# Performance work log

Measured on AMD Instinct MI355X. Metric: run time of the kernel, lower is better.

The kernel has to match this reference:

```python
import jax, jax.numpy as jnp
import numpy as np

B, NQ, NK = 16, 1024, 1024
DQ = DK = DV = 512
H = 4
DH = DV // H  # 128


def layer_norm(x, g, b, eps=1e-5):
    mu = jnp.mean(x, axis=-1, keepdims=True)
    var = jnp.var(x, axis=-1, keepdims=True)  # biased, matches torch LayerNorm
    return (x - mu) / jnp.sqrt(var + eps) * g + b


def setup_inputs() -> dict:
    key = jax.random.key(0)
    ks = jax.random.split(key, 16)
    s = lambda d: 1.0 / np.sqrt(d)
    return {
        "Q": jax.random.normal(ks[0], (B, NQ, DQ), jnp.float32),
        "K": jax.random.normal(ks[1], (B, NK, DK), jnp.float32),
        "weights": jax.random.uniform(ks[2], (H * B, NQ, NK), jnp.float32),
        "Wq": jax.random.normal(ks[3], (DV, DQ), jnp.float32) * s(DQ),
        "bq": jnp.zeros((DV,), jnp.float32),
        "Wk": jax.random.normal(ks[4], (DV, DK), jnp.float32) * s(DK),
        "bk": jnp.zeros((DV,), jnp.float32),
        "Wv": jax.random.normal(ks[5], (DV, DK), jnp.float32) * s(DK),
        "bv": jnp.zeros((DV,), jnp.float32),
        "Wo": jax.random.normal(ks[6], (DV, DV), jnp.float32) * s(DV),
        "bo": jnp.zeros((DV,), jnp.float32),
        "g0": jnp.ones((DV,), jnp.float32),
        "beta0": jnp.zeros((DV,), jnp.float32),
        "g1": jnp.ones((DV,), jnp.float32),
        "beta1": jnp.zeros((DV,), jnp.float32),
    }


def reference(Q, K, weights, Wq, bq, Wk, bk, Wv, bv, Wo, bo, g0, beta0, g1, beta1):
    q = Q @ Wq.T + bq  # [B,NQ,DV]
    k = K @ Wk.T + bk  # [B,NK,DV]
    v = K @ Wv.T + bv  # [B,NK,DV]

    # torch split(dh, 2) + cat(0) == head-major [H,B,N,DH]
    def heads(x, n):
        return x.reshape(B, n, H, DH).transpose(2, 0, 1, 3)

    q_, k_, v_ = heads(q, NQ), heads(k, NK), heads(v, NK)

    # NOTE: original scales by sqrt(dim_V), not sqrt(head_dim)
    scores = jnp.einsum("hbqd,hbkd->hbqk", q_, k_) / np.sqrt(DV)
    log_w = jnp.log(jnp.clip(weights, 0.0, None)).reshape(H, B, NQ, NK)
    A = jax.nn.softmax(scores + log_w, axis=-1)  # [H,B,NQ,NK]

    o = q_ + jnp.einsum("hbqk,hbkd->hbqd", A, v_)  # residual inside heads
    # split(B,0)+cat(2) == merge heads back to [B,NQ,DV]
    O = o.transpose(1, 2, 0, 3).reshape(B, NQ, DV)
    O = layer_norm(O, g0, beta0)
    O = O + jax.nn.relu(O @ Wo.T + bo)
    O = layer_norm(O, g1, beta1)
    return O
```

## Files before the change

kernel.cpp:

```cpp
#include <hip/hip_runtime.h>

typedef unsigned short u16;
typedef unsigned int u32;
typedef __attribute__((ext_vector_type(8))) short short8;
typedef __attribute__((ext_vector_type(4))) float f32x4;
typedef __attribute__((ext_vector_type(2))) u32 uintx2;
typedef __attribute__((address_space(3))) u32 lds32;
typedef const __attribute__((address_space(1))) u32 g32c;

__device__ __forceinline__ u16 f2bf(float f) {
  union { float f; u32 u; } v; v.f = f;
  return (u16)((v.u + 0x7fffu + ((v.u >> 16) & 1u)) >> 16);
}
__device__ __forceinline__ float bf2f(u16 h) {
  union { u32 u; float f; } v; v.u = ((u32)h) << 16;
  return v.f;
}

__global__ void cvt_w_kernel(const float* __restrict__ Wq, const float* __restrict__ Wk,
                             const float* __restrict__ Wv, const float* __restrict__ Wo,
                             u16* __restrict__ dst) {
  int m = blockIdx.y;
  const float* s = (m == 0) ? Wq : (m == 1) ? Wk : (m == 2) ? Wv : Wo;
  int idx = (blockIdx.x * 256 + threadIdx.x) * 4;
  float4 v = *(const float4*)(s + idx);
  uintx2 pk;
  pk[0] = (u32)f2bf(v.x) | ((u32)f2bf(v.y) << 16);
  pk[1] = (u32)f2bf(v.z) | ((u32)f2bf(v.w) << 16);
  *(uintx2*)(dst + m * 262144 + idx) = pk;
}

template <bool AF32, bool OUTMODE, bool TRANSV>
__device__ __forceinline__ void gemm_bt_body(const void* __restrict__ Ap,
                                             const u16* __restrict__ Bw,
                                             const float* __restrict__ bias,
                                             u16* __restrict__ C) {
  __shared__ u16 ldsA[128 * 64];
  __shared__ u16 ldsB[128 * 64];
  const int t = threadIdx.x;
  const int lane = t & 63, wid = t >> 6;
  const int lr = lane & 15, lg = lane >> 4;
  const int n0 = blockIdx.x * 128;
  const int m0 = blockIdx.y * 128;
  const int wr = (wid >> 1) * 64, wc = (wid & 1) * 64;

  f32x4 acc[4][4];
#pragma unroll
  for (int i = 0; i < 4; ++i)
#pragma unroll
    for (int j = 0; j < 4; ++j)
#pragma unroll
      for (int r = 0; r < 4; ++r) acc[i][j][r] = 0.f;

  for (int kt = 0; kt < 512; kt += 64) {
    __syncthreads();
#pragma unroll
    for (int i = 0; i < 4; ++i) {
      int lin = i * 256 + t;
      int row = lin >> 3, u = lin & 7;
      int pu = u ^ (row & 7);
      if constexpr (AF32) {
        const float* src = (const float*)Ap + (size_t)(m0 + row) * 512 + kt + u * 8;
        float4 v0 = *(const float4*)src;
        float4 v1 = *(const float4*)(src + 4);
        short8 pk;
        pk[0] = (short)f2bf(v0.x); pk[1] = (short)f2bf(v0.y);
        pk[2] = (short)f2bf(v0.z); pk[3] = (short)f2bf(v0.w);
        pk[4] = (short)f2bf(v1.x); pk[5] = (short)f2bf(v1.y);
        pk[6] = (short)f2bf(v1.z); pk[7] = (short)f2bf(v1.w);
        *(short8*)&ldsA[row * 64 + pu * 8] = pk;
      } else {
        const u16* src = (const u16*)Ap + (size_t)(m0 + row) * 512 + kt + u * 8;
        *(short8*)&ldsA[row * 64 + pu * 8] = *(const short8*)src;
      }
      const u16* bsrc = Bw + (size_t)(n0 + row) * 512 + kt + u * 8;
      *(short8*)&ldsB[row * 64 + pu * 8] = *(const short8*)bsrc;
    }
    __syncthreads();
#pragma unroll
    for (int kk = 0; kk < 2; ++kk) {
      short8 af[4], bfr[4];
#pragma unroll
      for (int mf = 0; mf < 4; ++mf) {
        int row = wr + mf * 16 + lr;
        af[mf] = *(const short8*)&ldsA[row * 64 + (((kk * 4 + lg) ^ (row & 7)) * 8)];
      }
#pragma unroll
      for (int nf = 0; nf < 4; ++nf) {
        int row = wc + nf * 16 + lr;
        bfr[nf] = *(const short8*)&ldsB[row * 64 + (((kk * 4 + lg) ^ (row & 7)) * 8)];
      }
#pragma unroll
      for (int mf = 0; mf < 4; ++mf)
#pragma unroll
        for (int nf = 0; nf < 4; ++nf)
          acc[mf][nf] =
              __builtin_amdgcn_mfma_f32_16x16x32_bf16(af[mf], bfr[nf], acc[mf][nf], 0, 0, 0);
    }
  }

  if constexpr (TRANSV) {
    const int h_ = n0 >> 7;
#pragma unroll
    for (int mf = 0; mf < 4; ++mf)
#pragma unroll
      for (int nf = 0; nf < 4; ++nf) {
        int d = wc + nf * 16 + lr;
        int rr0 = m0 + wr + mf * 16 + lg * 4;
        int b_ = rr0 >> 10;
        int k0 = rr0 & 1023;
        float bvv = bias[n0 + d];
        uintx2 pk;
        pk[0] = (u32)f2bf(acc[mf][nf][0] + bvv) | ((u32)f2bf(acc[mf][nf][1] + bvv) << 16);
        pk[1] = (u32)f2bf(acc[mf][nf][2] + bvv) | ((u32)f2bf(acc[mf][nf][3] + bvv) << 16);
        *(uintx2*)(C + (((size_t)b_ * 4 + h_) * 128 + d) * 1024 + k0) = pk;
      }
  } else {
#pragma unroll
    for (int mf = 0; mf < 4; ++mf)
#pragma unroll
      for (int nf = 0; nf < 4; ++nf) {
        int c = n0 + wc + nf * 16 + lr;
        float bv = bias[c];
#pragma unroll
        for (int r = 0; r < 4; ++r) {
          int rr = m0 + wr + mf * 16 + lg * 4 + r;
          float v = acc[mf][nf][r] + bv;
          if constexpr (OUTMODE) {
            v = v > 0.f ? v : 0.f;
            v += bf2f(((const u16*)Ap)[(size_t)rr * 512 + c]);
          }
          C[(size_t)rr * 512 + c] = f2bf(v);
        }
      }
  }
}

__global__ __launch_bounds__(256) void gemm3_kernel(const float* __restrict__ Q,
                                                    const float* __restrict__ K,
                                                    const u16* __restrict__ Wb,
                                                    const float* __restrict__ bq,
                                                    const float* __restrict__ bk,
                                                    const float* __restrict__ bv,
                                                    u16* qb, u16* kb, u16* vbT) {
  int z = blockIdx.z;
  if (z == 2) {
    gemm_bt_body<true, false, true>(K, Wb + 524288, bv, vbT);
  } else {
    const void* Ap = (z == 0) ? (const void*)Q : (const void*)K;
    const u16* Bw = Wb + z * 262144;
    const float* bias = (z == 0) ? bq : bk;
    u16* C = (z == 0) ? qb : kb;
    gemm_bt_body<true, false, false>(Ap, Bw, bias, C);
  }
}

__global__ __launch_bounds__(256) void gemmo_kernel(const u16* __restrict__ X,
                                                    const u16* __restrict__ Wb,
                                                    const float* __restrict__ bo,
                                                    u16* Z) {
  gemm_bt_body<false, true, false>(X, Wb, bo, Z);
}

__global__ __launch_bounds__(256, 3) void attn_kernel(const u16* __restrict__ qb,
                                                      const u16* __restrict__ kb,
                                                      const u16* __restrict__ vbT,
                                                      const float* __restrict__ Wt,
                                                      u16* __restrict__ Ob) {
  __shared__ __align__(16) u16 ldsK[2][32 * 128];
  __shared__ __align__(16) u16 ldsVT[2][128 * 32];
  __shared__ __align__(16) u16 ldsP[64 * 40];
  const int t = threadIdx.x;
  const int lane = t & 63, wid = t >> 6;
  const int lr = lane & 15, lg = lane >> 4;
  const int hb = blockIdx.y;
  const int b = hb & 15;
  const int h = hb >> 4;
  const int q0 = blockIdx.x * 64;
  const int wq = wid * 16;
  const size_t kvbase = ((size_t)b * 1024) * 512 + h * 128;
  const size_t vtbase = ((size_t)b * 4 + h) * 131072;
  const float SCALE = 0.044194173824159216f;

  const u16* ksrc[2];
  const u16* vtsrc[2];
#pragma unroll
  for (int i = 0; i < 2; ++i) {
    {
      int lin = i * 256 + t;
      int row = lin >> 4, u = lin & 15;
      ksrc[i] = kb + kvbase + (size_t)row * 512 + ((u ^ (row & 15)) * 8);
    }
    {
      int lin = i * 256 + t;
      int row = lin >> 2, u = lin & 3;
      vtsrc[i] = vbT + vtbase + (size_t)row * 1024 + ((u ^ (row & 3)) * 8);
    }
  }
  const int wslot = (t & 192) * 8;

#define STAGE(bu)                                                                           \
  do {                                                                                      \
    _Pragma("unroll") for (int i_ = 0; i_ < 2; ++i_) {                                      \
      __builtin_amdgcn_global_load_lds((g32c*)(ksrc[i_]),                                   \
                                       (lds32*)(&ldsK[bu][i_ * 2048 + wslot]), 16, 0, 0);   \
      __builtin_amdgcn_global_load_lds((g32c*)(vtsrc[i_]),                                  \
                                       (lds32*)(&ldsVT[bu][i_ * 2048 + wslot]), 16, 0, 0);  \
      ksrc[i_] += 16384;                                                \
      vtsrc[i_] += 32;                                                  \
    }                                                                                       \
  } while (0)

  const float* wp = Wt + ((size_t)hb * 1024 + q0 + wq + lr) * 1024 + lg * 4;

#define WLOADP(W)                        \
  do {                                   \
    W[0] = *(const f32x4*)(wp);          \
    W[1] = *(const f32x4*)(wp + 16);     \
    wp += 32;                            \
  } while (0)

  short8 qfr[4];
  {
    const u16* qp = qb + kvbase + (size_t)(q0 + wq + lr) * 512 + lg * 8;
#pragma unroll
    for (int ds = 0; ds < 4; ++ds) qfr[ds] = *(const short8*)(qp + ds * 32);
  }

  f32x4 oacc[8];
#pragma unroll
  for (int j = 0; j < 8; ++j)
#pragma unroll
    for (int r = 0; r < 4; ++r) oacc[j][r] = 0.f;
  float lacc = 0.f;

  auto tile_compute = [&](const u16* bK, const u16* bVT, const f32x4 (&W)[2]) {
    f32x4 sacc[2];
#pragma unroll
    for (int j = 0; j < 2; ++j)
#pragma unroll
      for (int r = 0; r < 4; ++r) sacc[j][r] = 0.f;

#pragma unroll
    for (int ds = 0; ds < 4; ++ds) {
      short8 kf[2];
#pragma unroll
      for (int mf = 0; mf < 2; ++mf) {
        int row = mf * 16 + lr;
        kf[mf] = *(const short8*)&bK[row * 128 + (((ds * 4 + lg) ^ (row & 15)) * 8)];
      }
      __builtin_amdgcn_s_setprio(1);
#pragma unroll
      for (int mf = 0; mf < 2; ++mf)
        sacc[mf] = __builtin_amdgcn_mfma_f32_16x16x32_bf16(kf[mf], qfr[ds], sacc[mf], 0, 0, 0);
      __builtin_amdgcn_s_setprio(0);
    }

    const int prow = wq + lr;
#pragma unroll
    for (int mf = 0; mf < 2; ++mf) {
      f32x4 w4 = W[mf];
      float p0 = w4[0] * __expf(sacc[mf][0] * SCALE);
      float p1 = w4[1] * __expf(sacc[mf][1] * SCALE);
      float p2 = w4[2] * __expf(sacc[mf][2] * SCALE);
      float p3 = w4[3] * __expf(sacc[mf][3] * SCALE);
      lacc += (p0 + p1) + (p2 + p3);
      uintx2 pk;
      pk[0] = (u32)f2bf(p0) | ((u32)f2bf(p1) << 16);
      pk[1] = (u32)f2bf(p2) | ((u32)f2bf(p3) << 16);
      *(uintx2*)((char*)ldsP + prow * 80 + mf * 32 + lg * 8) = pk;
    }

    short8 pa = *(const short8*)((const char*)ldsP + (wq + lr) * 80 + lg * 16);
    short8 vf[8];
#pragma unroll
    for (int nf = 0; nf < 8; ++nf) {
      int row = nf * 16 + lr;
      vf[nf] = *(const short8*)&bVT[row * 32 + ((lg ^ (row & 3)) * 8)];
    }
    __builtin_amdgcn_s_setprio(1);
#pragma unroll
    for (int nf = 0; nf < 8; ++nf)
      oacc[nf] = __builtin_amdgcn_mfma_f32_16x16x32_bf16(pa, vf[nf], oacc[nf], 0, 0, 0);
    __builtin_amdgcn_s_setprio(0);
  };

#define SCHED_FENCE() __builtin_amdgcn_sched_barrier(0)
#define WAITBAR(N)                                                 \
  do {                                                             \
    SCHED_FENCE();                                                 \
    asm volatile("s_waitcnt vmcnt(" #N ")" ::: "memory");          \
    __builtin_amdgcn_s_barrier();                                  \
    SCHED_FENCE();                                                 \
  } while (0)
#define BAR()                                                      \
  do {                                                             \
    SCHED_FENCE();                                                 \
    __builtin_amdgcn_s_barrier();                                  \
    SCHED_FENCE();                                                 \
  } while (0)

  f32x4 wA[2], wB[2];
  WLOADP(wA);
  STAGE(0);

  for (int it = 0; it < 16; ++it) {
    {
      STAGE(1);
      WLOADP(wB);
      WAITBAR(6);
      tile_compute(&ldsK[0][0], &ldsVT[0][0], wA);
      BAR();
    }
    {
      if (it < 15) {
        STAGE(0);
        WLOADP(wA);
        WAITBAR(6);
      } else {
        WAITBAR(0);
      }
      tile_compute(&ldsK[1][0], &ldsVT[1][0], wB);
      if (it < 15) BAR();
    }
  }

  float lred = lacc;
  lred += __shfl_xor(lred, 16);
  lred += __shfl_xor(lred, 32);

#pragma unroll
  for (int r = 0; r < 4; ++r) {
    float lv = __shfl(lred, (lane & 48) | (lg * 4 + r));
    float linv = 1.0f / lv;
    int qrow = q0 + wq + lg * 4 + r;
    size_t base = kvbase + (size_t)qrow * 512;
#pragma unroll
    for (int nf = 0; nf < 8; ++nf) {
      size_t idx = base + nf * 16 + lr;
      Ob[idx] = f2bf(bf2f(qb[idx]) + oacc[nf][r] * linv);
    }
  }
#undef STAGE
#undef WLOADP
#undef WAITBAR
#undef BAR
#undef SCHED_FENCE
}

template <bool F32OUT>
__global__ __launch_bounds__(256) void ln_kernel(const u16* __restrict__ in,
                                                 const float* __restrict__ g,
                                                 const float* __restrict__ be,
                                                 void* __restrict__ outp) {
  const int lane = threadIdx.x & 63, wid = threadIdx.x >> 6;
  const int row = blockIdx.x * 4 + wid;
  const u16* p = in + (size_t)row * 512 + lane * 8;
  short8 v = *(const short8*)p;
  float x[8];
  float s = 0.f, s2 = 0.f;
#pragma unroll
  for (int j = 0; j < 8; ++j) {
    x[j] = bf2f((u16)v[j]);
    s += x[j];
    s2 += x[j] * x[j];
  }
#pragma unroll
  for (int off = 1; off < 64; off <<= 1) {
    s += __shfl_xor(s, off);
    s2 += __shfl_xor(s2, off);
  }
  float mu = s * (1.f / 512.f);
  float var = s2 * (1.f / 512.f) - mu * mu;
  float rs = rsqrtf(var + 1e-5f);
  float4 ga = *(const float4*)(g + lane * 8);
  float4 gb = *(const float4*)(g + lane * 8 + 4);
  float4 ba = *(const float4*)(be + lane * 8);
  float4 bb = *(const float4*)(be + lane * 8 + 4);
  float gg[8] = {ga.x, ga.y, ga.z, ga.w, gb.x, gb.y, gb.z, gb.w};
  float bv[8] = {ba.x, ba.y, ba.z, ba.w, bb.x, bb.y, bb.z, bb.w};
  if constexpr (F32OUT) {
    float* out = (float*)outp + (size_t)row * 512 + lane * 8;
    float4 o0, o1;
    o0.x = (x[0] - mu) * rs * gg[0] + bv[0];
    o0.y = (x[1] - mu) * rs * gg[1] + bv[1];
    o0.z = (x[2] - mu) * rs * gg[2] + bv[2];
    o0.w = (x[3] - mu) * rs * gg[3] + bv[3];
    o1.x = (x[4] - mu) * rs * gg[4] + bv[4];
    o1.y = (x[5] - mu) * rs * gg[5] + bv[5];
    o1.z = (x[6] - mu) * rs * gg[6] + bv[6];
    o1.w = (x[7] - mu) * rs * gg[7] + bv[7];
    *(float4*)out = o0;
    *(float4*)(out + 4) = o1;
  } else {
    short8 o;
#pragma unroll
    for (int j = 0; j < 8; ++j) o[j] = (short)f2bf((x[j] - mu) * rs * gg[j] + bv[j]);
    *(short8*)((u16*)outp + (size_t)row * 512 + lane * 8) = o;
  }
}

extern "C" void kernel_launch(void* const* d_in, const int* in_sizes, int n_in,
                              void* d_out, int out_size, void* d_ws, size_t ws_size,
                              hipStream_t stream) {
  (void)in_sizes; (void)n_in; (void)out_size; (void)ws_size;
  const float* Q   = (const float*)d_in[0];
  const float* K   = (const float*)d_in[1];
  const float* Wt  = (const float*)d_in[2];
  const float* Wq  = (const float*)d_in[3];
  const float* bq  = (const float*)d_in[4];
  const float* Wk  = (const float*)d_in[5];
  const float* bk  = (const float*)d_in[6];
  const float* Wv  = (const float*)d_in[7];
  const float* bv  = (const float*)d_in[8];
  const float* Wo  = (const float*)d_in[9];
  const float* bo  = (const float*)d_in[10];
  const float* g0  = (const float*)d_in[11];
  const float* be0 = (const float*)d_in[12];
  const float* g1  = (const float*)d_in[13];
  const float* be1 = (const float*)d_in[14];

  char* ws = (char*)d_ws;
  const size_t MB16 = 16777216;
  u16* qb  = (u16*)(ws);
  u16* kb  = (u16*)(ws + MB16);
  u16* vbT = (u16*)(ws + 2 * MB16);
  u16* Wb  = (u16*)(ws + 3 * MB16);
  u16* Ob  = (u16*)d_out;

  cvt_w_kernel<<<dim3(256, 4), 256, 0, stream>>>(Wq, Wk, Wv, Wo, Wb);
  gemm3_kernel<<<dim3(4, 128, 3), 256, 0, stream>>>(Q, K, Wb, bq, bk, bv, qb, kb, vbT);
  attn_kernel<<<dim3(16, 64), 256, 0, stream>>>(qb, kb, vbT, Wt, Ob);
  ln_kernel<false><<<4096, 256, 0, stream>>>(Ob, g0, be0, qb);
  gemmo_kernel<<<dim3(4, 128), 256, 0, stream>>>(qb, Wb + 786432, bo, kb);
  ln_kernel<true><<<4096, 256, 0, stream>>>(kb, g1, be1, d_out);
}
```

Before: 258.1 us.

## Double attention KV tile to 64 and load V fragments directly to registers

The attention kernel now processes 64 keys per tile instead of 32, which halves the number of loop iterations and barriers. V^T fragments are read straight from global memory into registers instead of being staged through LDS. The P buffer in LDS is widened and XOR-swizzled to avoid bank conflicts. Each wave now loads the same V data redundantly and holds 16 extra short8 registers for it, which raises register pressure under the 3-blocks-per-SM launch bound and leans on the cache to absorb the duplicate V loads.

```diff
diff --git a/kernel.cpp b/kernel.cpp
--- a/kernel.cpp
+++ b/kernel.cpp
@@ -167,9 +167,8 @@
                                                       const u16* __restrict__ vbT,
                                                       const float* __restrict__ Wt,
                                                       u16* __restrict__ Ob) {
-  __shared__ __align__(16) u16 ldsK[2][32 * 128];
-  __shared__ __align__(16) u16 ldsVT[2][128 * 32];
-  __shared__ __align__(16) u16 ldsP[64 * 40];
+  __shared__ __align__(16) u16 ldsK[2][64 * 128];
+  __shared__ __align__(16) u16 ldsP[64 * 64];
   const int t = threadIdx.x;
   const int lane = t & 63, wid = t >> 6;
   const int lr = lane & 15, lg = lane >> 4;
@@ -182,43 +181,35 @@
   const size_t vtbase = ((size_t)b * 4 + h) * 131072;
   const float SCALE = 0.044194173824159216f;
 
-  const u16* ksrc[2];
-  const u16* vtsrc[2];
-#pragma unroll
-  for (int i = 0; i < 2; ++i) {
-    {
-      int lin = i * 256 + t;
-      int row = lin >> 4, u = lin & 15;
-      ksrc[i] = kb + kvbase + (size_t)row * 512 + ((u ^ (row & 15)) * 8);
-    }
-    {
-      int lin = i * 256 + t;
-      int row = lin >> 2, u = lin & 3;
-      vtsrc[i] = vbT + vtbase + (size_t)row * 1024 + ((u ^ (row & 3)) * 8);
-    }
+  const u16* ksrc[4];
+#pragma unroll
+  for (int i = 0; i < 4; ++i) {
+    int lin = i * 256 + t;
+    int row = lin >> 4, u = lin & 15;
+    ksrc[i] = kb + kvbase + (size_t)row * 512 + ((u ^ (row & 15)) * 8);
   }
   const int wslot = (t & 192) * 8;
 
-#define STAGE(bu)                                                                           \
-  do {                                                                                      \
-    _Pragma("unroll") for (int i_ = 0; i_ < 2; ++i_) {                                      \
-      __builtin_amdgcn_global_load_lds((g32c*)(ksrc[i_]),                                   \
-                                       (lds32*)(&ldsK[bu][i_ * 2048 + wslot]), 16, 0, 0);   \
-      __builtin_amdgcn_global_load_lds((g32c*)(vtsrc[i_]),                                  \
-                                       (lds32*)(&ldsVT[bu][i_ * 2048 + wslot]), 16, 0, 0);  \
-      ksrc[i_] += 16384;                                                \
-      vtsrc[i_] += 32;                                                  \
-    }                                                                                       \
+#define STAGE(bu)                                                                          \
+  do {                                                                                     \
+    _Pragma("unroll") for (int i_ = 0; i_ < 4; ++i_) {                                     \
+      __builtin_amdgcn_global_load_lds((g32c*)(ksrc[i_]),                                  \
+                                       (lds32*)(&ldsK[bu][i_ * 2048 + wslot]), 16, 0, 0);  \
+      ksrc[i_] += 32768;                                               \
+    }                                                                                      \
   } while (0)
 
   const float* wp = Wt + ((size_t)hb * 1024 + q0 + wq + lr) * 1024 + lg * 4;
 
-#define WLOADP(W)                        \
-  do {                                   \
-    W[0] = *(const f32x4*)(wp);          \
-    W[1] = *(const f32x4*)(wp + 16);     \
-    wp += 32;                            \
+#define WLOADP(W)                                      \
+  do {                                                 \
+    _Pragma("unroll") for (int m_ = 0; m_ < 4; ++m_) { \
+      W[m_] = *(const f32x4*)(wp + m_ * 16);           \
+    }                                                  \
+    wp += 64;                                          \
   } while (0)
+
+  const u16* vfbase = vbT + vtbase + (size_t)lr * 1024 + lg * 8;
 
   short8 qfr[4];
   {
@@ -234,31 +225,31 @@
     for (int r = 0; r < 4; ++r) oacc[j][r] = 0.f;
   float lacc = 0.f;
 
-  auto tile_compute = [&](const u16* bK, const u16* bVT, const f32x4 (&W)[2]) {
-    f32x4 sacc[2];
-#pragma unroll
-    for (int j = 0; j < 2; ++j)
+  auto tile_compute = [&](const u16* bK, const short8 (&vf)[16], const f32x4 (&W)[4]) {
+    f32x4 sacc[4];
+#pragma unroll
+    for (int j = 0; j < 4; ++j)
 #pragma unroll
       for (int r = 0; r < 4; ++r) sacc[j][r] = 0.f;
 
 #pragma unroll
     for (int ds = 0; ds < 4; ++ds) {
-      short8 kf[2];
-#pragma unroll
-      for (int mf = 0; mf < 2; ++mf) {
+      short8 kf[4];
+#pragma unroll
+      for (int mf = 0; mf < 4; ++mf) {
         int row = mf * 16 + lr;
         kf[mf] = *(const short8*)&bK[row * 128 + (((ds * 4 + lg) ^ (row & 15)) * 8)];
       }
       __builtin_amdgcn_s_setprio(1);
 #pragma unroll
-      for (int mf = 0; mf < 2; ++mf)
+      for (int mf = 0; mf < 4; ++mf)
         sacc[mf] = __builtin_amdgcn_mfma_f32_16x16x32_bf16(kf[mf], qfr[ds], sacc[mf], 0, 0, 0);
       __builtin_amdgcn_s_setprio(0);
     }
 
     const int prow = wq + lr;
 #pragma unroll
-    for (int mf = 0; mf < 2; ++mf) {
+    for (int mf = 0; mf < 4; ++mf) {
       f32x4 w4 = W[mf];
       float p0 = w4[0] * __expf(sacc[mf][0] * SCALE);
       float p1 = w4[1] * __expf(sacc[mf][1] * SCALE);
@@ -268,21 +259,21 @@
       uintx2 pk;
       pk[0] = (u32)f2bf(p0) | ((u32)f2bf(p1) << 16);
       pk[1] = (u32)f2bf(p2) | ((u32)f2bf(p3) << 16);
-      *(uintx2*)((char*)ldsP + prow * 80 + mf * 32 + lg * 8) = pk;
-    }
-
-    short8 pa = *(const short8*)((const char*)ldsP + (wq + lr) * 80 + lg * 16);
-    short8 vf[8];
-#pragma unroll
-    for (int nf = 0; nf < 8; ++nf) {
-      int row = nf * 16 + lr;
-      vf[nf] = *(const short8*)&bVT[row * 32 + ((lg ^ (row & 3)) * 8)];
-    }
-    __builtin_amdgcn_s_setprio(1);
-#pragma unroll
-    for (int nf = 0; nf < 8; ++nf)
-      oacc[nf] = __builtin_amdgcn_mfma_f32_16x16x32_bf16(pa, vf[nf], oacc[nf], 0, 0, 0);
-    __builtin_amdgcn_s_setprio(0);
+      int byteoff = (prow * 128 + (mf * 16 + lg * 4) * 2) ^ ((prow & 7) << 4);
+      *(uintx2*)((char*)ldsP + byteoff) = pk;
+    }
+
+#pragma unroll
+    for (int ks = 0; ks < 2; ++ks) {
+      int byteoff = (prow * 128 + (ks * 32 + lg * 8) * 2) ^ ((prow & 7) << 4);
+      short8 pa = *(const short8*)((const char*)ldsP + byteoff);
+      __builtin_amdgcn_s_setprio(1);
+#pragma unroll
+      for (int nf = 0; nf < 8; ++nf)
+        oacc[nf] =
+            __builtin_amdgcn_mfma_f32_16x16x32_bf16(pa, vf[ks * 8 + nf], oacc[nf], 0, 0, 0);
+      __builtin_amdgcn_s_setprio(0);
+    }
   };
 
 #define SCHED_FENCE() __builtin_amdgcn_sched_barrier(0)
@@ -300,28 +291,41 @@
     SCHED_FENCE();                                                 \
   } while (0)
 
-  f32x4 wA[2], wB[2];
+#define VFLOAD(vf, kt)                                                              \
+  do {                                                                              \
+    _Pragma("unroll") for (int ks_ = 0; ks_ < 2; ++ks_)                             \
+        _Pragma("unroll") for (int nf_ = 0; nf_ < 8; ++nf_) {                       \
+      vf[ks_ * 8 + nf_] =                                                           \
+          *(const short8*)(vfbase + (size_t)nf_ * 16384 + (kt) + ks_ * 32);         \
+    }                                                                               \
+  } while (0)
+
+  f32x4 wA[4], wB[4];
   WLOADP(wA);
   STAGE(0);
 
-  for (int it = 0; it < 16; ++it) {
+  for (int it = 0; it < 8; ++it) {
     {
+      short8 vf[16];
+      VFLOAD(vf, 2 * it * 64);
       STAGE(1);
       WLOADP(wB);
-      WAITBAR(6);
-      tile_compute(&ldsK[0][0], &ldsVT[0][0], wA);
+      WAITBAR(24);
+      tile_compute(&ldsK[0][0], vf, wA);
       BAR();
     }
     {
-      if (it < 15) {
+      short8 vf[16];
+      VFLOAD(vf, (2 * it + 1) * 64);
+      if (it < 7) {
         STAGE(0);
         WLOADP(wA);
-        WAITBAR(6);
+        WAITBAR(24);
       } else {
-        WAITBAR(0);
-      }
-      tile_compute(&ldsK[1][0], &ldsVT[1][0], wB);
-      if (it < 15) BAR();
+        WAITBAR(16);
+      }
+      tile_compute(&ldsK[1][0], vf, wB);
+      if (it < 7) BAR();
     }
   }
 
@@ -343,6 +347,7 @@
   }
 #undef STAGE
 #undef WLOADP
+#undef VFLOAD
 #undef WAITBAR
 #undef BAR
 #undef SCHED_FENCE
```

Result: slower. 659.5 us (+155.5%).
